# Kernel tuning notes

Measured on AMD Instinct MI355X. Metric: run time of the kernel, lower is better.

The kernel has to match this reference:

```python
import jax, jax.numpy as jnp
import numpy as np

N, E = 30000, 480000
D_IN, D_HID = 128, 256
NODE_CLS, EDGE_CLS, POLAR = 5, 2, 6
EPS = 1e-5

def layer_norm(x, g, b):
    mu = jnp.mean(x, axis=-1, keepdims=True)
    var = jnp.mean((x - mu) ** 2, axis=-1, keepdims=True)
    return g * (x - mu) / jnp.sqrt(var + EPS) + b

def sage_pool(h, src, dst, Wp, bp, Ws, bs, Wn, n_nodes):
    # DGL SAGEConv aggregator_type='pool': m = relu(fc_pool(h_src)); max over in-edges
    m = jax.nn.relu(h @ Wp + bp)              # [N, d_in]
    agg = jax.ops.segment_max(m[src], dst, num_segments=n_nodes)  # [N, d_in], -inf if no in-edges
    deg = jax.ops.segment_sum(jnp.ones((src.shape[0],), jnp.float32), dst, num_segments=n_nodes)
    h_neigh = jnp.where(deg[:, None] > 0, agg, 0.0)
    out = h @ Ws + bs + h_neigh @ Wn          # fc_self + fc_neigh
    return jax.nn.relu(out)                   # activation=F.relu

def setup_inputs() -> dict:
    key = jax.random.key(0)
    ks = jax.random.split(key, 24)
    p = lambda k, shape, fan: jax.random.normal(k, shape, jnp.float32) / np.sqrt(fan)
    return {
        "h": jax.random.normal(ks[0], (N, D_IN), jnp.float32),
        "efeat": jax.random.normal(ks[1], (E, POLAR), jnp.float32),
        "src": jax.random.randint(ks[2], (E,), 0, N, jnp.int32),
        "dst": jax.random.randint(ks[3], (E,), 0, N, jnp.int32),
        # encoder SAGEConv(128->256)
        "enc_Wpool": p(ks[4], (D_IN, D_IN), D_IN), "enc_bpool": jnp.zeros((D_IN,), jnp.float32),
        "enc_Wself": p(ks[5], (D_IN, D_HID), D_IN), "enc_bself": jnp.zeros((D_HID,), jnp.float32),
        "enc_Wneigh": p(ks[6], (D_IN, D_HID), D_IN),
        # node_pred: Linear(256,5) + LayerNorm(5)
        "np_W": p(ks[7], (D_HID, NODE_CLS), D_HID), "np_b": jnp.zeros((NODE_CLS,), jnp.float32),
        "np_g": jnp.ones((NODE_CLS,), jnp.float32), "np_beta": jnp.zeros((NODE_CLS,), jnp.float32),
        # edge predictor: Linear(528,256) + LN(256) + Linear(256,2)
        "ep_W1": p(ks[8], (2 * D_HID + 2 * NODE_CLS + POLAR, D_HID), 2 * D_HID + 16),
        "ep_b1": jnp.zeros((D_HID,), jnp.float32),
        "ep_g": jnp.ones((D_HID,), jnp.float32), "ep_beta": jnp.zeros((D_HID,), jnp.float32),
        "ep_W2": p(ks[9], (D_HID, EDGE_CLS), D_HID), "ep_b2": jnp.zeros((EDGE_CLS,), jnp.float32),
        # decoder SAGEConv(256->128)
        "dec_Wpool": p(ks[10], (D_HID, D_HID), D_HID), "dec_bpool": jnp.zeros((D_HID,), jnp.float32),
        "dec_Wself": p(ks[11], (D_HID, D_IN), D_HID), "dec_bself": jnp.zeros((D_IN,), jnp.float32),
        "dec_Wneigh": p(ks[12], (D_HID, D_IN), D_HID),
    }

def reference(h, efeat, src, dst,
              enc_Wpool, enc_bpool, enc_Wself, enc_bself, enc_Wneigh,
              np_W, np_b, np_g, np_beta,
              ep_W1, ep_b1, ep_g, ep_beta, ep_W2, ep_b2,
              dec_Wpool, dec_bpool, dec_Wself, dec_bself, dec_Wneigh):
    # encoder (drop_rate == 0 path)
    h1 = sage_pool(h, src, dst, enc_Wpool, enc_bpool, enc_Wself, enc_bself, enc_Wneigh, N)
    # node head
    node_pred = layer_norm(h1 @ np_W + np_b, np_g, np_beta)  # [N, 5]
    # edge head: gather-concat-MLP per edge
    cls_sm = jax.nn.softmax(node_pred, axis=1)               # softmax once, gather per edge
    x = jnp.concatenate([h1[src], cls_sm[src], efeat, h1[dst], cls_sm[dst]], axis=1)  # [E, 528]
    x = jax.nn.relu(layer_norm(x @ ep_W1 + ep_b1, ep_g, ep_beta))
    edges_pred = x @ ep_W2 + ep_b2                           # dropout is identity in eval
    # decoder (uses original graph, input h1)
    h2 = sage_pool(h1, src, dst, dec_Wpool, dec_bpool, dec_Wself, dec_bself, dec_Wneigh, N)
    return (node_pred, edges_pred, h2)
```

## Files before the change

kernel.cpp:

```cpp
#include <hip/hip_runtime.h>

typedef unsigned short u16;
typedef unsigned int u32;
typedef __bf16 bf16_t;
typedef bf16_t bf16x8 __attribute__((ext_vector_type(8)));
typedef float f32x4 __attribute__((ext_vector_type(4)));

#define N_NODES 30000
#define N_EDGES 480000

static __device__ __forceinline__ float b2f(u16 u) {
  return __uint_as_float(((u32)u) << 16);
}
static __device__ __forceinline__ float b2f_lo(u32 w) {
  return __uint_as_float(w << 16);
}
static __device__ __forceinline__ float b2f_hi(u32 w) {
  return __uint_as_float(w & 0xffff0000u);
}
static __device__ __forceinline__ u16 f2b(float f) {
  u32 x = __float_as_uint(f);
  u32 r = (x + 0x7fffu + ((x >> 16) & 1u)) >> 16;
  return (u16)r;
}

__global__ __launch_bounds__(256) void init_sniff_deg(const u16* __restrict__ h,
                                                      int* __restrict__ flag,
                                                      int* __restrict__ deg) {
  int i = blockIdx.x * 256 + threadIdx.x;
  if (i < N_NODES) deg[i] = 0;
  if (blockIdx.x == 0) {
    int t = threadIdx.x;
    int bad = 0;
#pragma unroll
    for (int j = 0; j < 4; j++) {
      u32 e = ((u32)h[t * 4 + j] >> 7) & 0xFFu;
      if (e >= 0x8Eu) bad = 1;
    }
    int r = __syncthreads_or(bad);
    if (t == 0) *flag = r ? 1 : 0;
  }
}

struct ConvDesc { const void* s; u16* d; int n; int off; };
struct ConvTab { ConvDesc e[20]; int total; };

__global__ __launch_bounds__(256) void conv_all(
    const int* __restrict__ dstE, int* __restrict__ deg,
    const void* __restrict__ hsrc, u16* __restrict__ c_h,
    const void* __restrict__ efsrc, u16* __restrict__ c_ef,
    ConvTab tab, const int* __restrict__ flag) {
  int b = blockIdx.x;
  const int t = threadIdx.x;
  if (b < 1875) {
    int e = b * 256 + t;
    if (e < N_EDGES) atomicAdd(&deg[dstE[e]], 1);
    return;
  }
  b -= 1875;
  const int f = *flag;
  if (b < 3750) {
    int i = b * 256 + t;
    if (f) {
      float4 v = ((const float4*)hsrc)[i];
      uint2 o;
      o.x = (u32)f2b(v.x) | ((u32)f2b(v.y) << 16);
      o.y = (u32)f2b(v.z) | ((u32)f2b(v.w) << 16);
      ((uint2*)c_h)[i] = o;
    } else {
      ((uint2*)c_h)[i] = ((const uint2*)hsrc)[i];
    }
    return;
  }
  b -= 3750;
  if (b < 2813) {
    int i = b * 256 + t;
    if (i < 720000) {
      if (f) {
        float4 v = ((const float4*)efsrc)[i];
        uint2 o;
        o.x = (u32)f2b(v.x) | ((u32)f2b(v.y) << 16);
        o.y = (u32)f2b(v.z) | ((u32)f2b(v.w) << 16);
        ((uint2*)c_ef)[i] = o;
      } else {
        ((uint2*)c_ef)[i] = ((const uint2*)efsrc)[i];
      }
    }
    return;
  }
  b -= 2813;
  int i = b * 256 + t;
  if (i >= tab.total) return;
#pragma unroll 1
  for (int a = 0; a < 20; a++) {
    int j = i - tab.e[a].off;
    if (j >= 0 && j < tab.e[a].n) {
      if (f) tab.e[a].d[j] = f2b(((const float*)tab.e[a].s)[j]);
      else tab.e[a].d[j] = ((const u16*)tab.e[a].s)[j];
      return;
    }
  }
}

__global__ __launch_bounds__(1024) void scan_off(const int* __restrict__ deg,
                                                 int* __restrict__ off,
                                                 int* __restrict__ cursor, int n) {
  __shared__ int carry;
  __shared__ int wsum[16];
  int t = threadIdx.x, lane = t & 63, wv = t >> 6;
  if (t == 0) { carry = 0; off[0] = 0; }
  __syncthreads();
  for (int base = 0; base < n; base += 1024) {
    int v = (base + t < n) ? deg[base + t] : 0;
    int x = v;
#pragma unroll
    for (int d = 1; d < 64; d <<= 1) {
      int y = __shfl_up(x, d, 64);
      if (lane >= d) x += y;
    }
    if (lane == 63) wsum[wv] = x;
    __syncthreads();
    int wadd = 0;
    for (int w = 0; w < wv; w++) wadd += wsum[w];
    int incl = x + wadd + carry;
    if (base + t < n) { off[base + t + 1] = incl; cursor[base + t] = incl - v; }
    __syncthreads();
    if (t == 1023) carry = incl;
    __syncthreads();
  }
}

__global__ __launch_bounds__(256) void fill_csr(const int* __restrict__ src,
                                                const int* __restrict__ dst,
                                                int* __restrict__ cursor,
                                                int* __restrict__ esrc, int nE) {
  int e = blockIdx.x * 256 + threadIdx.x;
  if (e >= nE) return;
  int p = atomicAdd(&cursor[dst[e]], 1);
  esrc[p] = src[e];
}

__global__ __launch_bounds__(256) void agg128(const u16* __restrict__ m,
                                              const int* __restrict__ esrc,
                                              const int* __restrict__ off,
                                              u16* __restrict__ out) {
  int wv = threadIdx.x >> 6, lane = threadIdx.x & 63;
  int qd = lane >> 4, l = lane & 15;
  int n = blockIdx.x * 16 + wv * 4 + qd;
  if (n >= N_NODES) return;
  int i = off[n], s1 = off[n + 1];
  u32 a0 = 0, a1 = 0, a2 = 0, a3 = 0, a4 = 0, a5 = 0, a6 = 0, a7 = 0;
  for (; i + 1 < s1; i += 2) {
    int e0 = esrc[i], e1 = esrc[i + 1];
    uint4 r0 = *(const uint4*)(m + (size_t)e0 * 128 + l * 8);
    uint4 r1 = *(const uint4*)(m + (size_t)e1 * 128 + l * 8);
    a0 = max(a0, r0.x & 0xffffu); a1 = max(a1, r0.x >> 16);
    a2 = max(a2, r0.y & 0xffffu); a3 = max(a3, r0.y >> 16);
    a4 = max(a4, r0.z & 0xffffu); a5 = max(a5, r0.z >> 16);
    a6 = max(a6, r0.w & 0xffffu); a7 = max(a7, r0.w >> 16);
    a0 = max(a0, r1.x & 0xffffu); a1 = max(a1, r1.x >> 16);
    a2 = max(a2, r1.y & 0xffffu); a3 = max(a3, r1.y >> 16);
    a4 = max(a4, r1.z & 0xffffu); a5 = max(a5, r1.z >> 16);
    a6 = max(a6, r1.w & 0xffffu); a7 = max(a7, r1.w >> 16);
  }
  if (i < s1) {
    uint4 r0 = *(const uint4*)(m + (size_t)esrc[i] * 128 + l * 8);
    a0 = max(a0, r0.x & 0xffffu); a1 = max(a1, r0.x >> 16);
    a2 = max(a2, r0.y & 0xffffu); a3 = max(a3, r0.y >> 16);
    a4 = max(a4, r0.z & 0xffffu); a5 = max(a5, r0.z >> 16);
    a6 = max(a6, r0.w & 0xffffu); a7 = max(a7, r0.w >> 16);
  }
  uint4 w;
  w.x = a0 | (a1 << 16); w.y = a2 | (a3 << 16);
  w.z = a4 | (a5 << 16); w.w = a6 | (a7 << 16);
  *(uint4*)(out + (size_t)n * 128 + l * 8) = w;
}

__global__ __launch_bounds__(256) void agg256(const u16* __restrict__ m,
                                              const int* __restrict__ esrc,
                                              const int* __restrict__ off,
                                              u16* __restrict__ out) {
  int wv = threadIdx.x >> 6, lane = threadIdx.x & 63;
  int half = lane >> 5, l = lane & 31;
  int n = blockIdx.x * 8 + wv * 2 + half;
  if (n >= N_NODES) return;
  int i = off[n], s1 = off[n + 1];
  u32 a0 = 0, a1 = 0, a2 = 0, a3 = 0, a4 = 0, a5 = 0, a6 = 0, a7 = 0;
  for (; i + 1 < s1; i += 2) {
    int e0 = esrc[i], e1 = esrc[i + 1];
    uint4 r0 = *(const uint4*)(m + (size_t)e0 * 256 + l * 8);
    uint4 r1 = *(const uint4*)(m + (size_t)e1 * 256 + l * 8);
    a0 = max(a0, r0.x & 0xffffu); a1 = max(a1, r0.x >> 16);
    a2 = max(a2, r0.y & 0xffffu); a3 = max(a3, r0.y >> 16);
    a4 = max(a4, r0.z & 0xffffu); a5 = max(a5, r0.z >> 16);
    a6 = max(a6, r0.w & 0xffffu); a7 = max(a7, r0.w >> 16);
    a0 = max(a0, r1.x & 0xffffu); a1 = max(a1, r1.x >> 16);
    a2 = max(a2, r1.y & 0xffffu); a3 = max(a3, r1.y >> 16);
    a4 = max(a4, r1.z & 0xffffu); a5 = max(a5, r1.z >> 16);
    a6 = max(a6, r1.w & 0xffffu); a7 = max(a7, r1.w >> 16);
  }
  if (i < s1) {
    uint4 r0 = *(const uint4*)(m + (size_t)esrc[i] * 256 + l * 8);
    a0 = max(a0, r0.x & 0xffffu); a1 = max(a1, r0.x >> 16);
    a2 = max(a2, r0.y & 0xffffu); a3 = max(a3, r0.y >> 16);
    a4 = max(a4, r0.z & 0xffffu); a5 = max(a5, r0.z >> 16);
    a6 = max(a6, r0.w & 0xffffu); a7 = max(a7, r0.w >> 16);
  }
  uint4 w;
  w.x = a0 | (a1 << 16); w.y = a2 | (a3 << 16);
  w.z = a4 | (a5 << 16); w.w = a6 | (a7 << 16);
  *(uint4*)(out + (size_t)n * 256 + l * 8) = w;
}

__global__ __launch_bounds__(256) void prep_weights(
    const u16* __restrict__ encWp, const u16* __restrict__ encWs, const u16* __restrict__ encWn,
    const u16* __restrict__ decWp, const u16* __restrict__ decWs, const u16* __restrict__ decWn,
    const u16* __restrict__ epW1, const u16* __restrict__ epb1,
    u16* __restrict__ wt_encpool, u16* __restrict__ wt_enc,
    u16* __restrict__ wt_decpool, u16* __restrict__ wt_dec,
    u16* __restrict__ wt_UV, u16* __restrict__ b512, float* __restrict__ swsum) {
  int b = blockIdx.x;
  const int t = threadIdx.x;
  if (b < 64) {
    int idx = b * 256 + t; int k = idx >> 7, n = idx & 127;
    wt_encpool[n * 128 + k] = encWp[k * 128 + n]; return;
  }
  b -= 64;
  if (b < 128) {
    int idx = b * 256 + t; int k = idx >> 8, n = idx & 255;
    wt_enc[n * 256 + k] = encWs[k * 256 + n]; return;
  }
  b -= 128;
  if (b < 128) {
    int idx = b * 256 + t; int k = idx >> 8, n = idx & 255;
    wt_enc[n * 256 + 128 + k] = encWn[k * 256 + n]; return;
  }
  b -= 128;
  if (b < 256) {
    int idx = b * 256 + t; int k = idx >> 8, n = idx & 255;
    wt_decpool[n * 256 + k] = decWp[k * 256 + n]; return;
  }
  b -= 256;
  if (b < 128) {
    int idx = b * 256 + t; int k = idx >> 7, n = idx & 127;
    wt_dec[n * 512 + k] = decWs[k * 128 + n]; return;
  }
  b -= 128;
  if (b < 128) {
    int idx = b * 256 + t; int k = idx >> 7, n = idx & 127;
    wt_dec[n * 512 + 256 + k] = decWn[k * 128 + n]; return;
  }
  b -= 128;
  if (b < 512) {
    int n = b, n2 = n & 255, base = (n >= 256) ? 267 : 0;
    for (int kp = t; kp < 288; kp += 256) {
      u16 v = (kp < 261) ? epW1[(size_t)(base + kp) * 256 + n2] : (u16)0;
      wt_UV[(size_t)n * 288 + kp] = v;
    }
    return;
  }
  b -= 512;
  if (b < 2) {
    int i = b * 256 + t;
    b512[i] = (i < 256) ? epb1[i] : (u16)0; return;
  }
  int k = t >> 5, l32 = t & 31;
  if (k < 6) {
    uint4 v = *(const uint4*)(epW1 + (size_t)(261 + k) * 256 + l32 * 8);
    float s = b2f_lo(v.x) + b2f_hi(v.x) + b2f_lo(v.y) + b2f_hi(v.y) +
              b2f_lo(v.z) + b2f_hi(v.z) + b2f_lo(v.w) + b2f_hi(v.w);
#pragma unroll
    for (int m = 1; m < 32; m <<= 1) s += __shfl_xor(s, m, 64);
    if (l32 == 0) swsum[k] = s;
  }
}

__global__ __launch_bounds__(256) void gemm_mfma(
    const u16* __restrict__ A0, const u16* __restrict__ A1, int K0, int K1,
    const u16* __restrict__ Bt, const u16* __restrict__ bias, int do_relu,
    u16* __restrict__ C, float* __restrict__ Cf, const int* __restrict__ flag,
    int M, int Nld) {
  __shared__ __align__(16) u16 As[128 * 40];
  __shared__ __align__(16) u16 Bs[128 * 40];
  const int t = threadIdx.x;
  const int lane = t & 63, wv = t >> 6;
  const int wm = wv & 1, wn = wv >> 1;
  const int r = lane & 15, q = lane >> 4;
  const int bm = blockIdx.x, bn = blockIdx.y;
  const int Ktot = K0 + K1;
  const bool usef = (Cf != nullptr) && (*flag != 0);

  f32x4 acc[4][4];
#pragma unroll
  for (int i = 0; i < 4; i++)
#pragma unroll
    for (int j = 0; j < 4; j++) acc[i][j] = (f32x4){0.f, 0.f, 0.f, 0.f};

  for (int kc = 0; kc < Ktot; kc += 32) {
#pragma unroll
    for (int h = 0; h < 2; h++) {
      int idx = t + h * 256;
      int rr = idx >> 2, qq = idx & 3;
      int rowg = bm * 128 + rr;
      uint4 av = make_uint4(0, 0, 0, 0);
      if (rowg < M) {
        const u16* p = (kc < K0) ? (A0 + (size_t)rowg * K0 + kc)
                                 : (A1 + (size_t)rowg * K1 + (kc - K0));
        av = *(const uint4*)(p + qq * 8);
      }
      *(uint4*)&As[rr * 40 + qq * 8] = av;
      int ng = bn * 128 + rr;
      uint4 bv = *(const uint4*)(Bt + (size_t)ng * Ktot + kc + qq * 8);
      *(uint4*)&Bs[rr * 40 + qq * 8] = bv;
    }
    __syncthreads();
    bf16x8 af[4], bfm[4];
#pragma unroll
    for (int mi = 0; mi < 4; mi++)
      af[mi] = *(const bf16x8*)&As[(wm * 64 + mi * 16 + r) * 40 + q * 8];
#pragma unroll
    for (int ni = 0; ni < 4; ni++)
      bfm[ni] = *(const bf16x8*)&Bs[(wn * 64 + ni * 16 + r) * 40 + q * 8];
#pragma unroll
    for (int mi = 0; mi < 4; mi++)
#pragma unroll
      for (int ni = 0; ni < 4; ni++)
        acc[mi][ni] = __builtin_amdgcn_mfma_f32_16x16x32_bf16(af[mi], bfm[ni], acc[mi][ni], 0, 0, 0);
    __syncthreads();
  }

  float bv[4];
#pragma unroll
  for (int ni = 0; ni < 4; ni++)
    bv[ni] = bias ? b2f(bias[bn * 128 + wn * 64 + ni * 16 + r]) : 0.f;
#pragma unroll
  for (int mi = 0; mi < 4; mi++) {
#pragma unroll
    for (int i = 0; i < 4; i++) {
      int rowg = bm * 128 + wm * 64 + mi * 16 + q * 4 + i;
      if (rowg >= M) continue;
#pragma unroll
      for (int ni = 0; ni < 4; ni++) {
        int colg = bn * 128 + wn * 64 + ni * 16 + r;
        float v = acc[mi][ni][i] + bv[ni];
        if (do_relu) v = v > 0.f ? v : 0.f;
        if (usef) Cf[(size_t)rowg * Nld + colg] = v;
        else C[(size_t)rowg * Nld + colg] = f2b(v);
      }
    }
  }
}

__global__ __launch_bounds__(256) void node_head(
    const u16* __restrict__ h1, const u16* __restrict__ W, const u16* __restrict__ b,
    const u16* __restrict__ g, const u16* __restrict__ beta,
    u16* __restrict__ outN, float* __restrict__ outNf, const int* __restrict__ flag,
    u16* __restrict__ smOut) {
  __shared__ float Wl[256 * 5];
  __shared__ float bl[5], gl[5], betal[5];
  int t = threadIdx.x;
#pragma unroll
  for (int c = 0; c < 5; c++) Wl[t * 5 + c] = b2f(W[t * 5 + c]);
  if (t < 5) { bl[t] = b2f(b[t]); gl[t] = b2f(g[t]); betal[t] = b2f(beta[t]); }
  __syncthreads();
  int n = blockIdx.x * 256 + t;
  if (n >= N_NODES) return;
  const bool usef = (*flag != 0);
  float acc[5] = {0.f, 0.f, 0.f, 0.f, 0.f};
  const u16* hp = h1 + (size_t)n * 256;
  for (int k8 = 0; k8 < 32; k8++) {
    uint4 v = *(const uint4*)(hp + k8 * 8);
    u32 wds[4] = {v.x, v.y, v.z, v.w};
#pragma unroll
    for (int h = 0; h < 4; h++) {
      float x0 = b2f_lo(wds[h]), x1 = b2f_hi(wds[h]);
      int k = k8 * 8 + h * 2;
#pragma unroll
      for (int c = 0; c < 5; c++)
        acc[c] += x0 * Wl[k * 5 + c] + x1 * Wl[(k + 1) * 5 + c];
    }
  }
  float x[5], mu = 0.f;
#pragma unroll
  for (int c = 0; c < 5; c++) { x[c] = acc[c] + bl[c]; mu += x[c]; }
  mu *= 0.2f;
  float var = 0.f;
#pragma unroll
  for (int c = 0; c < 5; c++) { float d = x[c] - mu; var += d * d; }
  var *= 0.2f;
  float rstd = rsqrtf(fmaxf(var, 0.f) + 1e-5f);
  float v5[5], mx = -1e30f;
#pragma unroll
  for (int c = 0; c < 5; c++) {
    v5[c] = gl[c] * (x[c] - mu) * rstd + betal[c];
    if (usef) outNf[(size_t)n * 5 + c] = v5[c];
    else outN[(size_t)n * 5 + c] = f2b(v5[c]);
    mx = fmaxf(mx, v5[c]);
  }
  float s = 0.f, ex[5];
#pragma unroll
  for (int c = 0; c < 5; c++) { ex[c] = __expf(v5[c] - mx); s += ex[c]; }
  float inv = 1.f / s;
  u16 row[32];
#pragma unroll
  for (int c = 0; c < 5; c++) row[c] = f2b(ex[c] * inv);
#pragma unroll
  for (int c = 5; c < 32; c++) row[c] = 0;
#pragma unroll
  for (int c = 0; c < 4; c++)
    *(uint4*)(smOut + (size_t)n * 32 + c * 8) = *(const uint4*)&row[c * 8];
}

__global__ __launch_bounds__(256) void rowsum_uv(const u16* __restrict__ UV,
                                                 float2* __restrict__ Srow) {
  int wv = threadIdx.x >> 6, lane = threadIdx.x & 63;
  int n = blockIdx.x * 4 + wv;
  if (n >= N_NODES) return;
  uint4 v = *(const uint4*)(UV + (size_t)n * 512 + lane * 8);
  float s = b2f_lo(v.x) + b2f_hi(v.x) + b2f_lo(v.y) + b2f_hi(v.y) +
            b2f_lo(v.z) + b2f_hi(v.z) + b2f_lo(v.w) + b2f_hi(v.w);
#pragma unroll
  for (int m = 1; m < 32; m <<= 1) s += __shfl_xor(s, m, 64);
  if (lane == 0) Srow[n].x = s;
  if (lane == 32) Srow[n].y = s;
}

__global__ __launch_bounds__(256) void edge_pt(
    const u16* __restrict__ UV, const float2* __restrict__ Srow,
    const float* __restrict__ swsum, const u16* __restrict__ ef,
    const int* __restrict__ src, const int* __restrict__ dst,
    const u16* __restrict__ w1raw,
    const u16* __restrict__ g, const u16* __restrict__ beta,
    const u16* __restrict__ w2, const u16* __restrict__ b2,
    u16* __restrict__ outE, float* __restrict__ outEf, const int* __restrict__ flag) {
  const int t = threadIdx.x;
  const int lane = t & 63, wv = t >> 6;
  const int c0 = lane * 4;
  const int grp = (lane >> 4) & 3;
  float wef[6][4], gl[4], bl[4], w20[4], w21[4];
#pragma unroll
  for (int k = 0; k < 6; k++) {
    u32 wa = *(const u32*)(w1raw + (size_t)(261 + k) * 256 + c0);
    u32 wb = *(const u32*)(w1raw + (size_t)(261 + k) * 256 + c0 + 2);
    wef[k][0] = b2f_lo(wa); wef[k][1] = b2f_hi(wa);
    wef[k][2] = b2f_lo(wb); wef[k][3] = b2f_hi(wb);
  }
#pragma unroll
  for (int j = 0; j < 4; j++) {
    gl[j] = b2f(g[c0 + j]); bl[j] = b2f(beta[c0 + j]);
    w20[j] = b2f(w2[(c0 + j) * 2]); w21[j] = b2f(w2[(c0 + j) * 2 + 1]);
  }
  float sw[6];
#pragma unroll
  for (int k = 0; k < 6; k++) sw[k] = swsum[k];
  const float b20 = b2f(b2[0]), b21 = b2f(b2[1]);
  const float bsel = (grp & 1) ? b21 : b20;
  const bool usef = (*flag != 0);

  const int pbase = (blockIdx.x * 4 + wv) * 16;
  int sa = src[pbase * 2], da = dst[pbase * 2];
  int sb = src[pbase * 2 + 1], db = dst[pbase * 2 + 1];
#pragma unroll 1
  for (int it = 0; it < 16; ++it) {
    const int e = (pbase + it) * 2;
    int sac = sa, dac = da, sbc = sb, dbc = db;
    if (it + 1 < 16) {
      sa = src[e + 2]; da = dst[e + 2]; sb = src[e + 3]; db = dst[e + 3];
    }
    uint2 ua = *(const uint2*)(UV + (size_t)sac * 512 + c0);
    uint2 va = *(const uint2*)(UV + (size_t)dac * 512 + 256 + c0);
    uint2 ub = *(const uint2*)(UV + (size_t)sbc * 512 + c0);
    uint2 vb = *(const uint2*)(UV + (size_t)dbc * 512 + 256 + c0);
    float2 sra = Srow[sac], srda = Srow[dac];
    float2 srb = Srow[sbc], srdb = Srow[dbc];
    const u32* efp = (const u32*)(ef + (size_t)e * 6);
    u32 f0 = efp[0], f1 = efp[1], f2 = efp[2], f3 = efp[3], f4 = efp[4], f5 = efp[5];
    float xa[6] = {b2f_lo(f0), b2f_hi(f0), b2f_lo(f1), b2f_hi(f1), b2f_lo(f2), b2f_hi(f2)};
    float xb[6] = {b2f_lo(f3), b2f_hi(f3), b2f_lo(f4), b2f_hi(f4), b2f_lo(f5), b2f_hi(f5)};

    float ma = sra.x + srda.y, mb = srb.x + srdb.y;
#pragma unroll
    for (int k = 0; k < 6; k++) { ma += xa[k] * sw[k]; mb += xb[k] * sw[k]; }
    ma *= (1.f / 256.f); mb *= (1.f / 256.f);

    float ya[4], yb[4];
    ya[0] = b2f_lo(ua.x) + b2f_lo(va.x); yb[0] = b2f_lo(ub.x) + b2f_lo(vb.x);
    ya[1] = b2f_hi(ua.x) + b2f_hi(va.x); yb[1] = b2f_hi(ub.x) + b2f_hi(vb.x);
    ya[2] = b2f_lo(ua.y) + b2f_lo(va.y); yb[2] = b2f_lo(ub.y) + b2f_lo(vb.y);
    ya[3] = b2f_hi(ua.y) + b2f_hi(va.y); yb[3] = b2f_hi(ub.y) + b2f_hi(vb.y);
#pragma unroll
    for (int k = 0; k < 6; k++)
#pragma unroll
      for (int j = 0; j < 4; j++) {
        ya[j] += xa[k] * wef[k][j];
        yb[j] += xb[k] * wef[k][j];
      }
    float pqa = ya[0] * ya[0] + ya[1] * ya[1] + ya[2] * ya[2] + ya[3] * ya[3];
    float pqb = yb[0] * yb[0] + yb[1] * yb[1] + yb[2] * yb[2] + yb[3] * yb[3];
    pqa += __shfl_xor(pqa, 32, 64);
    pqb += __shfl_xor(pqb, 32, 64);
    float z = (lane < 32) ? pqa : pqb;
#pragma unroll
    for (int m = 16; m >= 1; m >>= 1) z += __shfl_xor(z, m, 64);
    float zz = __shfl_xor(z, 32, 64);
    float pqa_t = (lane < 32) ? z : zz;
    float pqb_t = (lane < 32) ? zz : z;
    float rsa = rsqrtf(fmaxf(pqa_t * (1.f / 256.f) - ma * ma, 0.f) + 1e-5f);
    float rsb = rsqrtf(fmaxf(pqb_t * (1.f / 256.f) - mb * mb, 0.f) + 1e-5f);
    float p0a = 0.f, p1a = 0.f, p0b = 0.f, p1b = 0.f;
#pragma unroll
    for (int j = 0; j < 4; j++) {
      float na = fmaxf((ya[j] - ma) * rsa * gl[j] + bl[j], 0.f);
      float nb = fmaxf((yb[j] - mb) * rsb * gl[j] + bl[j], 0.f);
      p0a += na * w20[j]; p1a += na * w21[j];
      p0b += nb * w20[j]; p1b += nb * w21[j];
    }
    p0a += __shfl_xor(p0a, 32, 64); p1a += __shfl_xor(p1a, 32, 64);
    p0b += __shfl_xor(p0b, 32, 64); p1b += __shfl_xor(p1b, 32, 64);
    p0a += __shfl_xor(p0a, 16, 64); p1a += __shfl_xor(p1a, 16, 64);
    p0b += __shfl_xor(p0b, 16, 64); p1b += __shfl_xor(p1b, 16, 64);
    float w = (grp & 2) ? ((grp & 1) ? p1b : p0b) : ((grp & 1) ? p1a : p0a);
#pragma unroll
    for (int m = 8; m >= 1; m >>= 1) w += __shfl_xor(w, m, 64);
    if ((lane & 15) == 0) {
      float val = w + bsel;
      size_t oi = (size_t)e * 2 + grp;
      if (usef) outEf[oi] = val;
      else outE[oi] = f2b(val);
    }
  }
}

extern "C" void kernel_launch(void* const* d_in, const int* in_sizes, int n_in,
                              void* d_out, int out_size, void* d_ws, size_t ws_size,
                              hipStream_t stream) {
  char* wp = (char*)d_ws;
  auto alloc = [&](size_t bytes) -> char* {
    char* p = wp; wp += (bytes + 255) & ~(size_t)255; return p;
  };
  int* flag       = (int*)alloc(256);
  u16* c_h        = (u16*)alloc((size_t)N_NODES * 128 * 2);
  u16* c_ef       = (u16*)alloc((size_t)N_EDGES * 6 * 2);
  static const int pidx[20] = {4,5,6,7,8, 9,10,11,12, 13,14,15,16,17,18, 19,20,21,22,23};
  static const int pn[20]   = {16384,128,32768,256,32768, 1280,5,5,5,
                               135168,256,256,256,512,2, 65536,256,32768,128,32768};
  u16* cp[20];
  for (int a = 0; a < 20; a++) cp[a] = (u16*)alloc((size_t)pn[a] * 2);

  u16* wt_encpool = (u16*)alloc(128 * 128 * 2);
  u16* wt_enc     = (u16*)alloc(256 * 256 * 2);
  u16* wt_decpool = (u16*)alloc(256 * 256 * 2);
  u16* wt_dec     = (u16*)alloc(128 * 512 * 2);
  u16* wt_UV      = (u16*)alloc(512 * 288 * 2);
  u16* b512       = (u16*)alloc(512 * 2);
  float2* Srow    = (float2*)alloc((size_t)N_NODES * 8);
  float* swsum_b  = (float*)alloc(64);
  u16* m_buf      = (u16*)alloc((size_t)N_NODES * 256 * 2);
  u16* aggb       = (u16*)alloc((size_t)N_NODES * 256 * 2);
  u16* UVbuf      = m_buf;
  u16* h1b        = (u16*)alloc((size_t)N_NODES * 256 * 2);
  u16* smb32      = (u16*)alloc((size_t)N_NODES * 32 * 2);
  int* deg        = (int*)alloc((size_t)N_NODES * 4);
  int* off        = (int*)alloc((size_t)(N_NODES + 1) * 4);
  int* cursor     = (int*)alloc((size_t)N_NODES * 4);
  int* esrc       = (int*)alloc((size_t)N_EDGES * 4);

  const int* src = (const int*)d_in[2];
  const int* dst = (const int*)d_in[3];

  u16* outN = (u16*)d_out;
  u16* outE = outN + (size_t)N_NODES * 5;
  u16* outH = outN + 1110000;
  float* outNf = (float*)d_out;
  float* outEf = outNf + (size_t)N_NODES * 5;
  float* outHf = outNf + 1110000;

  init_sniff_deg<<<118, 256, 0, stream>>>((const u16*)d_in[0], flag, deg);
  ConvTab tab;
  int off_a = 0;
  for (int a = 0; a < 20; a++) {
    tab.e[a].s = d_in[pidx[a]]; tab.e[a].d = cp[a]; tab.e[a].n = pn[a]; tab.e[a].off = off_a;
    off_a += pn[a];
  }
  tab.total = off_a;
  int conv_blocks = 1875 + 3750 + 2813 + (off_a + 255) / 256;
  conv_all<<<conv_blocks, 256, 0, stream>>>(dst, deg, d_in[0], c_h, d_in[1], c_ef, tab, flag);

  const u16 *enc_Wpool = cp[0], *enc_bpool = cp[1], *enc_Wself = cp[2], *enc_bself = cp[3],
            *enc_Wneigh = cp[4], *np_W = cp[5], *np_b = cp[6], *np_g = cp[7], *np_beta = cp[8],
            *ep_W1 = cp[9], *ep_b1 = cp[10], *ep_g = cp[11], *ep_beta = cp[12],
            *ep_W2 = cp[13], *ep_b2 = cp[14], *dec_Wpool = cp[15], *dec_bpool = cp[16],
            *dec_Wself = cp[17], *dec_bself = cp[18], *dec_Wneigh = cp[19];

  scan_off<<<1, 1024, 0, stream>>>(deg, off, cursor, N_NODES);
  fill_csr<<<1875, 256, 0, stream>>>(src, dst, cursor, esrc, N_EDGES);

  prep_weights<<<1347, 256, 0, stream>>>(enc_Wpool, enc_Wself, enc_Wneigh,
                                         dec_Wpool, dec_Wself, dec_Wneigh,
                                         ep_W1, ep_b1,
                                         wt_encpool, wt_enc, wt_decpool, wt_dec,
                                         wt_UV, b512, swsum_b);

  gemm_mfma<<<dim3(235, 1), 256, 0, stream>>>(c_h, nullptr, 128, 0, wt_encpool,
                                              enc_bpool, 1, m_buf, nullptr, flag, N_NODES, 128);
  agg128<<<1875, 256, 0, stream>>>(m_buf, esrc, off, aggb);
  gemm_mfma<<<dim3(235, 2), 256, 0, stream>>>(c_h, aggb, 128, 128, wt_enc,
                                              enc_bself, 1, h1b, nullptr, flag, N_NODES, 256);
  node_head<<<118, 256, 0, stream>>>(h1b, np_W, np_b, np_g, np_beta, outN, outNf, flag, smb32);
  gemm_mfma<<<dim3(235, 4), 256, 0, stream>>>(h1b, smb32, 256, 32, wt_UV,
                                              b512, 0, UVbuf, nullptr, flag, N_NODES, 512);
  rowsum_uv<<<7500, 256, 0, stream>>>(UVbuf, Srow);
  edge_pt<<<3750, 256, 0, stream>>>(UVbuf, Srow, swsum_b, c_ef, src, dst, ep_W1,
                                    ep_g, ep_beta, ep_W2, ep_b2, outE, outEf, flag);
  gemm_mfma<<<dim3(235, 2), 256, 0, stream>>>(h1b, nullptr, 256, 0, wt_decpool,
                                              dec_bpool, 1, m_buf, nullptr, flag, N_NODES, 256);
  agg256<<<3750, 256, 0, stream>>>(m_buf, esrc, off, aggb);
  gemm_mfma<<<dim3(235, 1), 256, 0, stream>>>(h1b, aggb, 256, 256, wt_dec,
                                              dec_bself, 1, outH, outHf, flag, N_NODES, 128);
}
```

Before: 475.5 us.

## Precompute per-edge mean records in a separate pass and vectorize edge_pt math

Adds an edge_mean kernel that computes each edge pair's LayerNorm mean from Srow and edge features and packs indices, means and raw edge features into 48-byte uint4 records. edge_pt then reads one contiguous record stream with uniform (readfirstlane) addressing instead of separate src/dst/ef/Srow gathers. It also rewrites the per-lane arithmetic as float2 vector ops so packed FMA can be used. The cost is an extra launch plus writing and rereading about 11.5 MB of records.

```diff
diff --git a/kernel.cpp b/kernel.cpp
--- a/kernel.cpp
+++ b/kernel.cpp
@@ -5,6 +5,7 @@
 typedef __bf16 bf16_t;
 typedef bf16_t bf16x8 __attribute__((ext_vector_type(8)));
 typedef float f32x4 __attribute__((ext_vector_type(4)));
+typedef float f32x2 __attribute__((ext_vector_type(2)));
 
 #define N_NODES 30000
 #define N_EDGES 480000
@@ -425,10 +426,39 @@
   if (lane == 32) Srow[n].y = s;
 }
 
+__global__ __launch_bounds__(256) void edge_mean(
+    const int* __restrict__ src, const int* __restrict__ dst,
+    const u16* __restrict__ ef, const float2* __restrict__ Srow,
+    const float* __restrict__ swsum, uint4* __restrict__ recs) {
+  int p = blockIdx.x * 256 + threadIdx.x;
+  if (p >= 240000) return;
+  int e = p * 2;
+  int s0 = src[e], s1 = src[e + 1];
+  int d0 = dst[e], d1 = dst[e + 1];
+  const u32* efp = (const u32*)(ef + (size_t)e * 6);
+  u32 f0 = efp[0], f1 = efp[1], f2 = efp[2], f3 = efp[3], f4 = efp[4], f5 = efp[5];
+  float xa[6] = {b2f_lo(f0), b2f_hi(f0), b2f_lo(f1), b2f_hi(f1), b2f_lo(f2), b2f_hi(f2)};
+  float xb[6] = {b2f_lo(f3), b2f_hi(f3), b2f_lo(f4), b2f_hi(f4), b2f_lo(f5), b2f_hi(f5)};
+  float sw[6];
+#pragma unroll
+  for (int k = 0; k < 6; k++) sw[k] = swsum[k];
+  float m0 = Srow[s0].x + Srow[d0].y;
+  float m1 = Srow[s1].x + Srow[d1].y;
+#pragma unroll
+  for (int k = 0; k < 6; k++) { m0 += xa[k] * sw[k]; m1 += xb[k] * sw[k]; }
+  m0 *= (1.f / 256.f);
+  m1 *= (1.f / 256.f);
+  uint4 ra, rb, rc;
+  ra.x = (u32)s0; ra.y = (u32)d0; ra.z = (u32)s1; ra.w = (u32)d1;
+  rb.x = __float_as_uint(m0); rb.y = __float_as_uint(m1); rb.z = f0; rb.w = f1;
+  rc.x = f2; rc.y = f3; rc.z = f4; rc.w = f5;
+  recs[(size_t)p * 3 + 0] = ra;
+  recs[(size_t)p * 3 + 1] = rb;
+  recs[(size_t)p * 3 + 2] = rc;
+}
+
 __global__ __launch_bounds__(256) void edge_pt(
-    const u16* __restrict__ UV, const float2* __restrict__ Srow,
-    const float* __restrict__ swsum, const u16* __restrict__ ef,
-    const int* __restrict__ src, const int* __restrict__ dst,
+    const u16* __restrict__ UV, const uint4* __restrict__ recs,
     const u16* __restrict__ w1raw,
     const u16* __restrict__ g, const u16* __restrict__ beta,
     const u16* __restrict__ w2, const u16* __restrict__ b2,
@@ -437,66 +467,62 @@
   const int lane = t & 63, wv = t >> 6;
   const int c0 = lane * 4;
   const int grp = (lane >> 4) & 3;
-  float wef[6][4], gl[4], bl[4], w20[4], w21[4];
+  f32x2 wefA[6], wefB[6];
 #pragma unroll
   for (int k = 0; k < 6; k++) {
     u32 wa = *(const u32*)(w1raw + (size_t)(261 + k) * 256 + c0);
     u32 wb = *(const u32*)(w1raw + (size_t)(261 + k) * 256 + c0 + 2);
-    wef[k][0] = b2f_lo(wa); wef[k][1] = b2f_hi(wa);
-    wef[k][2] = b2f_lo(wb); wef[k][3] = b2f_hi(wb);
-  }
+    wefA[k] = (f32x2){b2f_lo(wa), b2f_hi(wa)};
+    wefB[k] = (f32x2){b2f_lo(wb), b2f_hi(wb)};
+  }
+  f32x2 glA = (f32x2){b2f(g[c0]), b2f(g[c0 + 1])};
+  f32x2 glB = (f32x2){b2f(g[c0 + 2]), b2f(g[c0 + 3])};
+  f32x2 blA = (f32x2){b2f(beta[c0]), b2f(beta[c0 + 1])};
+  f32x2 blB = (f32x2){b2f(beta[c0 + 2]), b2f(beta[c0 + 3])};
+  float w20[4], w21[4];
 #pragma unroll
   for (int j = 0; j < 4; j++) {
-    gl[j] = b2f(g[c0 + j]); bl[j] = b2f(beta[c0 + j]);
     w20[j] = b2f(w2[(c0 + j) * 2]); w21[j] = b2f(w2[(c0 + j) * 2 + 1]);
   }
-  float sw[6];
-#pragma unroll
-  for (int k = 0; k < 6; k++) sw[k] = swsum[k];
   const float b20 = b2f(b2[0]), b21 = b2f(b2[1]);
   const float bsel = (grp & 1) ? b21 : b20;
   const bool usef = (*flag != 0);
-
-  const int pbase = (blockIdx.x * 4 + wv) * 16;
-  int sa = src[pbase * 2], da = dst[pbase * 2];
-  int sb = src[pbase * 2 + 1], db = dst[pbase * 2 + 1];
+  const f32x2 zero2 = (f32x2){0.f, 0.f};
+
+  const int pb = __builtin_amdgcn_readfirstlane((blockIdx.x * 4 + wv) * 16);
+  const uint4* rp = recs + (size_t)pb * 3;
+  uint4 ra = rp[0], rb = rp[1], rc = rp[2];
 #pragma unroll 1
   for (int it = 0; it < 16; ++it) {
-    const int e = (pbase + it) * 2;
-    int sac = sa, dac = da, sbc = sb, dbc = db;
-    if (it + 1 < 16) {
-      sa = src[e + 2]; da = dst[e + 2]; sb = src[e + 3]; db = dst[e + 3];
-    }
-    uint2 ua = *(const uint2*)(UV + (size_t)sac * 512 + c0);
-    uint2 va = *(const uint2*)(UV + (size_t)dac * 512 + 256 + c0);
-    uint2 ub = *(const uint2*)(UV + (size_t)sbc * 512 + c0);
-    uint2 vb = *(const uint2*)(UV + (size_t)dbc * 512 + 256 + c0);
-    float2 sra = Srow[sac], srda = Srow[dac];
-    float2 srb = Srow[sbc], srdb = Srow[dbc];
-    const u32* efp = (const u32*)(ef + (size_t)e * 6);
-    u32 f0 = efp[0], f1 = efp[1], f2 = efp[2], f3 = efp[3], f4 = efp[4], f5 = efp[5];
-    float xa[6] = {b2f_lo(f0), b2f_hi(f0), b2f_lo(f1), b2f_hi(f1), b2f_lo(f2), b2f_hi(f2)};
-    float xb[6] = {b2f_lo(f3), b2f_hi(f3), b2f_lo(f4), b2f_hi(f4), b2f_lo(f5), b2f_hi(f5)};
-
-    float ma = sra.x + srda.y, mb = srb.x + srdb.y;
-#pragma unroll
-    for (int k = 0; k < 6; k++) { ma += xa[k] * sw[k]; mb += xb[k] * sw[k]; }
-    ma *= (1.f / 256.f); mb *= (1.f / 256.f);
-
-    float ya[4], yb[4];
-    ya[0] = b2f_lo(ua.x) + b2f_lo(va.x); yb[0] = b2f_lo(ub.x) + b2f_lo(vb.x);
-    ya[1] = b2f_hi(ua.x) + b2f_hi(va.x); yb[1] = b2f_hi(ub.x) + b2f_hi(vb.x);
-    ya[2] = b2f_lo(ua.y) + b2f_lo(va.y); yb[2] = b2f_lo(ub.y) + b2f_lo(vb.y);
-    ya[3] = b2f_hi(ua.y) + b2f_hi(va.y); yb[3] = b2f_hi(ub.y) + b2f_hi(vb.y);
-#pragma unroll
-    for (int k = 0; k < 6; k++)
-#pragma unroll
-      for (int j = 0; j < 4; j++) {
-        ya[j] += xa[k] * wef[k][j];
-        yb[j] += xb[k] * wef[k][j];
-      }
-    float pqa = ya[0] * ya[0] + ya[1] * ya[1] + ya[2] * ya[2] + ya[3] * ya[3];
-    float pqb = yb[0] * yb[0] + yb[1] * yb[1] + yb[2] * yb[2] + yb[3] * yb[3];
+    const int e = (pb + it) * 2;
+    uint4 ca = ra, cb = rb, cc = rc;
+    ra = rp[3 * it + 3]; rb = rp[3 * it + 4]; rc = rp[3 * it + 5];
+    const int s0 = (int)ca.x, d0 = (int)ca.y, s1 = (int)ca.z, d1 = (int)ca.w;
+    const float ma = __uint_as_float(cb.x), mb = __uint_as_float(cb.y);
+    float xa[6] = {b2f_lo(cb.z), b2f_hi(cb.z), b2f_lo(cb.w), b2f_hi(cb.w),
+                   b2f_lo(cc.x), b2f_hi(cc.x)};
+    float xb[6] = {b2f_lo(cc.y), b2f_hi(cc.y), b2f_lo(cc.z), b2f_hi(cc.z),
+                   b2f_lo(cc.w), b2f_hi(cc.w)};
+    uint2 ua = *(const uint2*)(UV + ((size_t)(u32)s0 << 9) + c0);
+    uint2 va = *(const uint2*)(UV + ((size_t)(u32)d0 << 9) + 256 + c0);
+    uint2 ub = *(const uint2*)(UV + ((size_t)(u32)s1 << 9) + c0);
+    uint2 vb = *(const uint2*)(UV + ((size_t)(u32)d1 << 9) + 256 + c0);
+
+    f32x2 yaA = (f32x2){b2f_lo(ua.x), b2f_hi(ua.x)} + (f32x2){b2f_lo(va.x), b2f_hi(va.x)};
+    f32x2 yaB = (f32x2){b2f_lo(ua.y), b2f_hi(ua.y)} + (f32x2){b2f_lo(va.y), b2f_hi(va.y)};
+    f32x2 ybA = (f32x2){b2f_lo(ub.x), b2f_hi(ub.x)} + (f32x2){b2f_lo(vb.x), b2f_hi(vb.x)};
+    f32x2 ybB = (f32x2){b2f_lo(ub.y), b2f_hi(ub.y)} + (f32x2){b2f_lo(vb.y), b2f_hi(vb.y)};
+#pragma unroll
+    for (int k = 0; k < 6; k++) {
+      yaA += xa[k] * wefA[k];
+      yaB += xa[k] * wefB[k];
+      ybA += xb[k] * wefA[k];
+      ybB += xb[k] * wefB[k];
+    }
+    float pqa = yaA.x * yaA.x;
+    pqa += yaA.y * yaA.y; pqa += yaB.x * yaB.x; pqa += yaB.y * yaB.y;
+    float pqb = ybA.x * ybA.x;
+    pqb += ybA.y * ybA.y; pqb += ybB.x * ybB.x; pqb += ybB.y * ybB.y;
     pqa += __shfl_xor(pqa, 32, 64);
     pqb += __shfl_xor(pqb, 32, 64);
     float z = (lane < 32) ? pqa : pqb;
@@ -507,14 +533,18 @@
     float pqb_t = (lane < 32) ? zz : z;
     float rsa = rsqrtf(fmaxf(pqa_t * (1.f / 256.f) - ma * ma, 0.f) + 1e-5f);
     float rsb = rsqrtf(fmaxf(pqb_t * (1.f / 256.f) - mb * mb, 0.f) + 1e-5f);
-    float p0a = 0.f, p1a = 0.f, p0b = 0.f, p1b = 0.f;
-#pragma unroll
-    for (int j = 0; j < 4; j++) {
-      float na = fmaxf((ya[j] - ma) * rsa * gl[j] + bl[j], 0.f);
-      float nb = fmaxf((yb[j] - mb) * rsb * gl[j] + bl[j], 0.f);
-      p0a += na * w20[j]; p1a += na * w21[j];
-      p0b += nb * w20[j]; p1b += nb * w21[j];
-    }
+    f32x2 nAa = __builtin_elementwise_max((yaA - ma) * rsa * glA + blA, zero2);
+    f32x2 nAb = __builtin_elementwise_max((yaB - ma) * rsa * glB + blB, zero2);
+    f32x2 nBa = __builtin_elementwise_max((ybA - mb) * rsb * glA + blA, zero2);
+    f32x2 nBb = __builtin_elementwise_max((ybB - mb) * rsb * glB + blB, zero2);
+    float p0a = nAa.x * w20[0], p1a = nAa.x * w21[0];
+    p0a += nAa.y * w20[1]; p1a += nAa.y * w21[1];
+    p0a += nAb.x * w20[2]; p1a += nAb.x * w21[2];
+    p0a += nAb.y * w20[3]; p1a += nAb.y * w21[3];
+    float p0b = nBa.x * w20[0], p1b = nBa.x * w21[0];
+    p0b += nBa.y * w20[1]; p1b += nBa.y * w21[1];
+    p0b += nBb.x * w20[2]; p1b += nBb.x * w21[2];
+    p0b += nBb.y * w20[3]; p1b += nBb.y * w21[3];
     p0a += __shfl_xor(p0a, 32, 64); p1a += __shfl_xor(p1a, 32, 64);
     p0b += __shfl_xor(p0b, 32, 64); p1b += __shfl_xor(p1b, 32, 64);
     p0a += __shfl_xor(p0a, 16, 64); p1a += __shfl_xor(p1a, 16, 64);
@@ -564,6 +594,7 @@
   int* off        = (int*)alloc((size_t)(N_NODES + 1) * 4);
   int* cursor     = (int*)alloc((size_t)N_NODES * 4);
   int* esrc       = (int*)alloc((size_t)N_EDGES * 4);
+  uint4* recs     = (uint4*)alloc(((size_t)240000 * 3 + 8) * 16);
 
   const int* src = (const int*)d_in[2];
   const int* dst = (const int*)d_in[3];
@@ -610,8 +641,9 @@
   gemm_mfma<<<dim3(235, 4), 256, 0, stream>>>(h1b, smb32, 256, 32, wt_UV,
                                               b512, 0, UVbuf, nullptr, flag, N_NODES, 512);
   rowsum_uv<<<7500, 256, 0, stream>>>(UVbuf, Srow);
-  edge_pt<<<3750, 256, 0, stream>>>(UVbuf, Srow, swsum_b, c_ef, src, dst, ep_W1,
-                                    ep_g, ep_beta, ep_W2, ep_b2, outE, outEf, flag);
+  edge_mean<<<938, 256, 0, stream>>>(src, dst, c_ef, Srow, swsum_b, recs);
+  edge_pt<<<3750, 256, 0, stream>>>(UVbuf, recs, ep_W1, ep_g, ep_beta, ep_W2, ep_b2,
+                                    outE, outEf, flag);
   gemm_mfma<<<dim3(235, 2), 256, 0, stream>>>(h1b, nullptr, 256, 0, wt_decpool,
                                               dec_bpool, 1, m_buf, nullptr, flag, N_NODES, 256);
   agg256<<<3750, 256, 0, stream>>>(m_buf, esrc, off, aggb);
```

Result: faster. 461.1 us, median of 2 (-3.0%).
